# Performance work log

Measured on AMD Instinct MI355X. Metric: run time of the kernel, lower is better.

The kernel has to match this reference:

```python
import jax, jax.numpy as jnp
import numpy as np

L2 = 15
L3 = 32
NUM_EXPERTS = 16
EXPERT_DIM = 2048
ROUTER_DIM = 128
B = 32768


def setup_inputs() -> dict:
    key = jax.random.key(0)
    ks = jax.random.split(key, 10)
    s = lambda fan_in: 1.0 / np.sqrt(fan_in)
    return {
        "expert_input": jax.random.normal(ks[0], (B, EXPERT_DIM), jnp.float32),
        "router_input": jax.random.normal(ks[1], (B, ROUTER_DIM), jnp.float32),
        "router_w": jax.random.normal(ks[2], (NUM_EXPERTS, ROUTER_DIM), jnp.float32) * 0.01,
        "router_b": jnp.zeros((NUM_EXPERTS,), jnp.float32),
        "l1_w": jax.random.uniform(ks[3], (NUM_EXPERTS, L2 + 1, EXPERT_DIM), jnp.float32, -s(EXPERT_DIM), s(EXPERT_DIM)),
        "l1_b": jax.random.uniform(ks[4], (NUM_EXPERTS, L2 + 1), jnp.float32, -s(EXPERT_DIM), s(EXPERT_DIM)),
        "l2_w": jax.random.uniform(ks[5], (NUM_EXPERTS, L3, 2 * L2), jnp.float32, -s(2 * L2), s(2 * L2)),
        "l2_b": jax.random.uniform(ks[6], (NUM_EXPERTS, L3), jnp.float32, -s(2 * L2), s(2 * L2)),
        "out_w": jax.random.uniform(ks[7], (NUM_EXPERTS, 1, L3), jnp.float32, -s(L3), s(L3)),
        "out_b": jnp.zeros((NUM_EXPERTS, 1), jnp.float32),
    }


def reference(expert_input, router_input, router_w, router_b, l1_w, l1_b, l2_w, l2_b, out_w, out_b):
    # Router (eval path: hard argmax routing)
    gate_logits = router_input @ router_w.T + router_b          # (B, E)
    expert_indices = jnp.argmax(gate_logits, axis=-1)           # (B,)

    # All-experts dense forward
    l1c = jnp.einsum('bi,eoi->beo', expert_input, l1_w) + l1_b  # (B, E, L2+1)
    l1x, l1x_out = l1c[..., :L2], l1c[..., L2:]                 # (B,E,L2), (B,E,1)
    l1x = jnp.clip(jnp.concatenate([jnp.square(l1x) * (255.0 / 256.0), l1x], axis=-1), 0.0, 1.0)  # (B,E,2*L2)
    l2c = jnp.einsum('bei,eoi->beo', l1x, l2_w) + l2_b          # (B, E, L3)
    l2x = jnp.clip(l2c, 0.0, 1.0)
    l3c = jnp.einsum('bei,eoi->beo', l2x, out_w) + out_b        # (B, E, 1)
    all_outputs = l3c + l1x_out                                 # (B, E, 1)

    # Gather the routed expert's output per token
    l3x = jnp.take_along_axis(all_outputs, expert_indices[:, None, None], axis=1)[:, 0, :]  # (B, 1)
    return l3x
```

## Files before the change

### kernel.cpp

```cpp
#include <hip/hip_runtime.h>

#define B_TOK 32768
#define EDIM 2048
#define RDIM 128
#define NEXP 16

__global__ __launch_bounds__(256) void k_router(
    const float* __restrict__ rin, const float* __restrict__ rw,
    const float* __restrict__ rb, int* __restrict__ counts,
    int* __restrict__ perm)
{
  __shared__ float lds[64 * 132];
  const int t = threadIdx.x;
  const int row0 = blockIdx.x * 64;

  {
    const int r = t >> 2;
    const int c0 = t & 3;
    const float4* src = (const float4*)(rin + (size_t)(row0 + r) * RDIM);
    float4* dst = (float4*)lds;
#pragma unroll
    for (int j = 0; j < 8; ++j) {
      const int f4 = c0 + 4 * j;
      dst[r * 33 + f4] = src[f4];
    }
  }
  __syncthreads();

  if (t < 64) {
    const int token = row0 + t;
    const float4* arow = (const float4*)lds + t * 33;
    double best = -1e300;
    int bi = 0;
#pragma unroll 1
    for (int e = 0; e < NEXP; ++e) {
      const float4* w = (const float4*)(rw + e * RDIM);
      double s = (double)rb[e];
#pragma unroll
      for (int i4 = 0; i4 < 32; ++i4) {
        const float4 a = arow[i4];
        const float4 ww = w[i4];
        s += (double)a.x * ww.x + (double)a.y * ww.y +
             (double)a.z * ww.z + (double)a.w * ww.w;
      }
      if (s > best) { best = s; bi = e; }
    }
    const int slot = atomicAdd(&counts[bi], 1);
    perm[bi * B_TOK + slot] = token;
  }
}

__global__ __launch_bounds__(256) void k_moe(
    const float* __restrict__ xin, const float* __restrict__ w1,
    const float* __restrict__ b1, const float* __restrict__ w2,
    const float* __restrict__ b2, const float* __restrict__ w3,
    const float* __restrict__ b3, const int* __restrict__ counts,
    const int* __restrict__ perm, float* __restrict__ out)
{
  const int e = blockIdx.y;
  const int n = counts[e];
  const int start = blockIdx.x * 64;
  if (start >= n) return;

  const int t = threadIdx.x;
  __shared__ float a_lds[64 * 132];
  __shared__ float c_lds[64 * 17];
  __shared__ int tok_lds[64];

  if (t < 64) {
    const int idx = start + t;
    tok_lds[t] = (idx < n) ? perm[e * B_TOK + idx] : -1;
  }
  __syncthreads();

  const int r = t >> 2;
  const int c0 = t & 3;
  const int tr = tok_lds[r];
  const float* srcrow = xin + (size_t)(tr < 0 ? 0 : tr) * EDIM;

  const int m = t & 63;
  const int og = __builtin_amdgcn_readfirstlane(t >> 6);
  const float* wbase = w1 + ((size_t)e * 16 + og * 4) * EDIM;

  float acc[4] = {0.f, 0.f, 0.f, 0.f};

  for (int kc = 0; kc < EDIM; kc += 128) {
    __syncthreads();
    {
      const float4* src = (const float4*)(srcrow + kc);
      float4* dst = (float4*)a_lds;
#pragma unroll
      for (int j = 0; j < 8; ++j) {
        const int f4 = c0 + 4 * j;
        dst[r * 33 + f4] = src[f4];
      }
    }
    __syncthreads();
    const float4* arow = (const float4*)(a_lds) + m * 33;
#pragma unroll
    for (int i4 = 0; i4 < 32; ++i4) {
      const float4 a = arow[i4];
#pragma unroll
      for (int o = 0; o < 4; ++o) {
        const float4 w = *(const float4*)(wbase + (size_t)o * EDIM + kc + i4 * 4);
        acc[o] = fmaf(a.x, w.x, acc[o]);
        acc[o] = fmaf(a.y, w.y, acc[o]);
        acc[o] = fmaf(a.z, w.z, acc[o]);
        acc[o] = fmaf(a.w, w.w, acc[o]);
      }
    }
  }

#pragma unroll
  for (int o = 0; o < 4; ++o)
    c_lds[m * 17 + og * 4 + o] = acc[o] + b1[e * 16 + og * 4 + o];
  __syncthreads();

  if (t < 64 && start + t < n) {
    const int token = tok_lds[t];
    const float* c = &c_lds[t * 17];
    const float xo = c[15];
    float x[30];
#pragma unroll
    for (int j = 0; j < 15; ++j) {
      const float v = c[j];
      x[j] = fminf(v * v * (255.0f / 256.0f), 1.0f);
      x[j + 15] = fminf(fmaxf(v, 0.0f), 1.0f);
    }
    const float* w2e = w2 + (size_t)e * 32 * 30;
    const float* b2e = b2 + e * 32;
    const float* w3e = w3 + e * 32;
    float acc3 = b3[e];
#pragma unroll 1
    for (int o2 = 0; o2 < 32; ++o2) {
      float s = b2e[o2];
#pragma unroll
      for (int i = 0; i < 30; ++i) s = fmaf(x[i], w2e[o2 * 30 + i], s);
      s = fminf(fmaxf(s, 0.0f), 1.0f);
      acc3 = fmaf(s, w3e[o2], acc3);
    }
    out[token] = acc3 + xo;
  }
}

extern "C" void kernel_launch(void* const* d_in, const int* in_sizes, int n_in,
                              void* d_out, int out_size, void* d_ws, size_t ws_size,
                              hipStream_t stream) {
  const float* xin = (const float*)d_in[0];
  const float* rin = (const float*)d_in[1];
  const float* rw  = (const float*)d_in[2];
  const float* rb  = (const float*)d_in[3];
  const float* w1  = (const float*)d_in[4];
  const float* b1  = (const float*)d_in[5];
  const float* w2  = (const float*)d_in[6];
  const float* b2  = (const float*)d_in[7];
  const float* w3  = (const float*)d_in[8];
  const float* b3  = (const float*)d_in[9];
  float* out = (float*)d_out;

  int* counts = (int*)d_ws;
  int* perm   = counts + 64;

  hipMemsetAsync(counts, 0, 64 * sizeof(int), stream);
  k_router<<<dim3(B_TOK / 64), 256, 0, stream>>>(rin, rw, rb, counts, perm);
  k_moe<<<dim3(B_TOK / 64, NEXP), 256, 0, stream>>>(xin, w1, b1, w2, b2, w3, b3,
                                                    counts, perm, out);
}
```

Baseline: 635.3 us.

## Stage expert weight tile in LDS and coalesce token row loads

The W1 slice for each K-chunk is now loaded cooperatively into shared memory, so each wave reads it from LDS instead of every thread issuing its own global/scalar loads per FMA group. Token rows are loaded with 32 lanes per row, giving fully coalesced 512-byte reads per row, and padding tokens now point to row 0 instead of being clamped. Launch bounds request 3 blocks per CU to bound register use. The cost is extra LDS traffic and footprint per block, which may limit occupancy.

```diff
diff --git a/kernel.cpp b/kernel.cpp
--- a/kernel.cpp
+++ b/kernel.cpp
@@ -4,6 +4,8 @@
 #define EDIM 2048
 #define RDIM 128
 #define NEXP 16
+#define BK 128
+#define XPITCH 33
 
 __global__ __launch_bounds__(256) void k_router(
     const float* __restrict__ rin, const float* __restrict__ rw,
@@ -50,7 +52,7 @@
   }
 }
 
-__global__ __launch_bounds__(256) void k_moe(
+__global__ __launch_bounds__(256, 3) void k_moe(
     const float* __restrict__ xin, const float* __restrict__ w1,
     const float* __restrict__ b1, const float* __restrict__ w2,
     const float* __restrict__ b2, const float* __restrict__ w3,
@@ -63,57 +65,75 @@
   if (start >= n) return;
 
   const int t = threadIdx.x;
-  __shared__ float a_lds[64 * 132];
-  __shared__ float c_lds[64 * 17];
-  __shared__ int tok_lds[64];
+  __shared__ float4 x_lds[64 * XPITCH];
+  __shared__ float4 w_lds[16 * 32];
+  __shared__ float  c_lds[64 * 17];
+  __shared__ int    tok_lds[64];
 
   if (t < 64) {
     const int idx = start + t;
-    tok_lds[t] = (idx < n) ? perm[e * B_TOK + idx] : -1;
+    tok_lds[t] = (idx < n) ? perm[e * B_TOK + idx] : 0;
   }
   __syncthreads();
 
-  const int r = t >> 2;
-  const int c0 = t & 3;
-  const int tr = tok_lds[r];
-  const float* srcrow = xin + (size_t)(tr < 0 ? 0 : tr) * EDIM;
+  const int srow  = t >> 5;
+  const int slane = t & 31;
+  const int m  = t & 63;
+  const int og = __builtin_amdgcn_readfirstlane(t >> 6);
 
-  const int m = t & 63;
-  const int og = __builtin_amdgcn_readfirstlane(t >> 6);
-  const float* wbase = w1 + ((size_t)e * 16 + og * 4) * EDIM;
+  const float* srcp[8];
+#pragma unroll
+  for (int rr = 0; rr < 8; ++rr)
+    srcp[rr] = xin + (size_t)tok_lds[srow + 8 * rr] * EDIM;
 
-  float acc[4] = {0.f, 0.f, 0.f, 0.f};
+  const float4* w1e = (const float4*)(w1 + (size_t)e * 16 * EDIM);
 
-  for (int kc = 0; kc < EDIM; kc += 128) {
+  float acc0 = 0.f, acc1 = 0.f, acc2 = 0.f, acc3 = 0.f;
+
+  for (int kc = 0; kc < EDIM; kc += BK) {
     __syncthreads();
-    {
-      const float4* src = (const float4*)(srcrow + kc);
-      float4* dst = (float4*)a_lds;
 #pragma unroll
-      for (int j = 0; j < 8; ++j) {
-        const int f4 = c0 + 4 * j;
-        dst[r * 33 + f4] = src[f4];
-      }
+    for (int rr = 0; rr < 8; ++rr) {
+      const int row = srow + 8 * rr;
+      x_lds[row * XPITCH + slane] =
+          ((const float4*)(srcp[rr] + kc))[slane];
+    }
+#pragma unroll
+    for (int q = 0; q < 2; ++q) {
+      const int idx = q * 256 + t;
+      const int o  = idx >> 5;
+      const int i4 = idx & 31;
+      w_lds[o * 32 + i4] = w1e[(size_t)o * (EDIM / 4) + (kc / 4) + i4];
     }
     __syncthreads();
-    const float4* arow = (const float4*)(a_lds) + m * 33;
+
+    const float4* xr = &x_lds[m * XPITCH];
+    const float4* wr = &w_lds[og * 4 * 32];
 #pragma unroll
     for (int i4 = 0; i4 < 32; ++i4) {
-      const float4 a = arow[i4];
-#pragma unroll
-      for (int o = 0; o < 4; ++o) {
-        const float4 w = *(const float4*)(wbase + (size_t)o * EDIM + kc + i4 * 4);
-        acc[o] = fmaf(a.x, w.x, acc[o]);
-        acc[o] = fmaf(a.y, w.y, acc[o]);
-        acc[o] = fmaf(a.z, w.z, acc[o]);
-        acc[o] = fmaf(a.w, w.w, acc[o]);
-      }
+      const float4 a  = xr[i4];
+      const float4 q0 = wr[i4];
+      const float4 q1 = wr[32 + i4];
+      const float4 q2 = wr[64 + i4];
+      const float4 q3 = wr[96 + i4];
+      acc0 = fmaf(a.x, q0.x, acc0); acc0 = fmaf(a.y, q0.y, acc0);
+      acc0 = fmaf(a.z, q0.z, acc0); acc0 = fmaf(a.w, q0.w, acc0);
+      acc1 = fmaf(a.x, q1.x, acc1); acc1 = fmaf(a.y, q1.y, acc1);
+      acc1 = fmaf(a.z, q1.z, acc1); acc1 = fmaf(a.w, q1.w, acc1);
+      acc2 = fmaf(a.x, q2.x, acc2); acc2 = fmaf(a.y, q2.y, acc2);
+      acc2 = fmaf(a.z, q2.z, acc2); acc2 = fmaf(a.w, q2.w, acc2);
+      acc3 = fmaf(a.x, q3.x, acc3); acc3 = fmaf(a.y, q3.y, acc3);
+      acc3 = fmaf(a.z, q3.z, acc3); acc3 = fmaf(a.w, q3.w, acc3);
     }
   }
 
-#pragma unroll
-  for (int o = 0; o < 4; ++o)
-    c_lds[m * 17 + og * 4 + o] = acc[o] + b1[e * 16 + og * 4 + o];
+  {
+    const float* b1e = b1 + e * 16 + og * 4;
+    c_lds[m * 17 + og * 4 + 0] = acc0 + b1e[0];
+    c_lds[m * 17 + og * 4 + 1] = acc1 + b1e[1];
+    c_lds[m * 17 + og * 4 + 2] = acc2 + b1e[2];
+    c_lds[m * 17 + og * 4 + 3] = acc3 + b1e[3];
+  }
   __syncthreads();
 
   if (t < 64 && start + t < n) {
@@ -124,22 +144,22 @@
 #pragma unroll
     for (int j = 0; j < 15; ++j) {
       const float v = c[j];
-      x[j] = fminf(v * v * (255.0f / 256.0f), 1.0f);
+      x[j]      = fminf(v * v * (255.0f / 256.0f), 1.0f);
       x[j + 15] = fminf(fmaxf(v, 0.0f), 1.0f);
     }
     const float* w2e = w2 + (size_t)e * 32 * 30;
     const float* b2e = b2 + e * 32;
     const float* w3e = w3 + e * 32;
-    float acc3 = b3[e];
+    float acc3v = b3[e];
 #pragma unroll 1
     for (int o2 = 0; o2 < 32; ++o2) {
       float s = b2e[o2];
 #pragma unroll
       for (int i = 0; i < 30; ++i) s = fmaf(x[i], w2e[o2 * 30 + i], s);
       s = fminf(fmaxf(s, 0.0f), 1.0f);
-      acc3 = fmaf(s, w3e[o2], acc3);
+      acc3v = fmaf(s, w3e[o2], acc3v);
     }
-    out[token] = acc3 + xo;
+    out[token] = acc3v + xo;
   }
 }
 
```

Result: slower. 656.6 us (+3.4%).
